# Optimization experiments

Measured on AMD Instinct MI355X. Metric: run time of the kernel, lower is better.

## Reference

```python
import jax, jax.numpy as jnp
import numpy as np

N_NODES = 50000
D = 128
N_EDGES = 600000


def setup_inputs() -> dict:
    key = jax.random.key(0)
    k_h, k_u, k_v, k_s, k_d = jax.random.split(key, 5)
    H = jax.random.normal(k_h, (N_NODES, D), dtype=jnp.float32)
    U = jax.random.normal(k_u, (D, D), dtype=jnp.float32)
    V = jax.random.normal(k_v, (D, D), dtype=jnp.float32)
    edge_src = jax.random.randint(k_s, (N_EDGES,), 0, N_NODES, dtype=jnp.int32)
    edge_dst = jax.random.randint(k_d, (N_EDGES,), 0, N_NODES, dtype=jnp.int32)
    return {"H": H, "U": U, "V": V, "edge_src": edge_src, "edge_dst": edge_dst}


def reference(H, U, V, edge_src, edge_dst):
    # Synchronous form of: new_rep[n] = relu(rep[n] @ U + sum_{m in N(n)} rep[m] @ V)
    # Compute H @ V once (one dense GEMM), then irregular gather by edge_src
    # and segment-sum scatter into destination nodes.
    hv = H @ V                                    # [N, D]
    msgs = jnp.take(hv, edge_src, axis=0)         # [E, D] irregular gather
    agg = jax.ops.segment_sum(msgs, edge_dst, num_segments=H.shape[0])  # [N, D]
    return jax.nn.relu(H @ U + agg)               # [N, D]
```

## Files before the change

### kernel.cpp

```cpp
#include <hip/hip_runtime.h>
#include <hip/hip_bf16.h>

constexpr int kNodes  = 50000;
constexpr int kEdges  = 600000;
constexpr int kD      = 128;
constexpr int kStrips = kNodes / 16;
constexpr int kStride = 64;
constexpr int kFillBlocks = (kEdges + 255) / 256;
constexpr int kPairBlocks = 2 * kFillBlocks;
constexpr int kTotalBlocks = kStrips + kFillBlocks;

typedef __attribute__((ext_vector_type(8))) short  short8;
typedef __attribute__((ext_vector_type(4))) float  f32x4;

__device__ __forceinline__ short f2bf(float x) {
    __hip_bfloat16 h = __float2bfloat16(x);
    return __builtin_bit_cast(short, h);
}

__global__ __launch_bounds__(512) void pack_init(const float* __restrict__ U,
                                                 const float* __restrict__ V,
                                                 short* __restrict__ BTf,
                                                 int* __restrict__ cursor) {
    const int g = blockIdx.x * 512 + threadIdx.x;
    if (g < 256 * kD) {
        const int c = g >> 7;
        const int k = g & 127;
        const float x = (c < kD) ? U[k * kD + c] : V[k * kD + (c - kD)];
        const int q  = c >> 6;
        const int n  = (c >> 4) & 3;
        const int m  = c & 15;
        const int t  = k >> 5;
        const int kg = (k >> 3) & 3;
        const int ko = k & 7;
        const int lane = kg * 16 + m;
        BTf[((((q * 4 + n) * 4 + t) * 64 + lane) << 3) + ko] = f2bf(x);
    }
    if (g < kNodes) cursor[g] = 0;
}

__global__ __launch_bounds__(256) void gemm_fill(const float* __restrict__ H,
                                                 const short* __restrict__ BTf,
                                                 const int* __restrict__ esrc,
                                                 const int* __restrict__ edst,
                                                 unsigned short* __restrict__ outb,
                                                 unsigned short* __restrict__ hvb,
                                                 int* __restrict__ cursor,
                                                 unsigned short* __restrict__ csr16) {
    const int bid = blockIdx.x;

    if (bid < kPairBlocks && (bid & 1)) {
        const int e = (bid >> 1) * 256 + (int)threadIdx.x;
        if (e < kEdges) {
            const int d = edst[e];
            const int slot = atomicAdd(&cursor[d], 1);
            if (slot < kStride)
                csr16[(size_t)d * kStride + slot] = (unsigned short)esrc[e];
        }
        return;
    }

    const int strip = (bid < kPairBlocks) ? (bid >> 1)
                                          : (kFillBlocks + (bid - kPairBlocks));
    const int quad  = threadIdx.x >> 6;
    const int lane  = threadIdx.x & 63;
    const int m  = lane & 15;
    const int kg = lane >> 4;
    const long row0 = (long)strip * 16;

    const float* hbase = H + (row0 + m) * kD + kg * 8;
    float4 ha[4][2];
#pragma unroll
    for (int t = 0; t < 4; ++t) {
        ha[t][0] = *reinterpret_cast<const float4*>(hbase + t * 32);
        ha[t][1] = *reinterpret_cast<const float4*>(hbase + t * 32 + 4);
    }

    const short8* bq = reinterpret_cast<const short8*>(BTf)
                     + ((size_t)quad * 16) * 64 + lane;
    short8 bf[4][4];
#pragma unroll
    for (int n = 0; n < 4; ++n)
#pragma unroll
        for (int t = 0; t < 4; ++t)
            bf[n][t] = bq[(n * 4 + t) * 64];

    short8 a[4];
#pragma unroll
    for (int t = 0; t < 4; ++t) {
        a[t][0] = f2bf(ha[t][0].x); a[t][1] = f2bf(ha[t][0].y);
        a[t][2] = f2bf(ha[t][0].z); a[t][3] = f2bf(ha[t][0].w);
        a[t][4] = f2bf(ha[t][1].x); a[t][5] = f2bf(ha[t][1].y);
        a[t][6] = f2bf(ha[t][1].z); a[t][7] = f2bf(ha[t][1].w);
    }

    f32x4 acc[4];
#pragma unroll
    for (int i = 0; i < 4; ++i) acc[i] = (f32x4){0.f, 0.f, 0.f, 0.f};
#pragma unroll
    for (int t = 0; t < 4; ++t)
#pragma unroll
        for (int n = 0; n < 4; ++n)
            acc[n] = __builtin_amdgcn_mfma_f32_16x16x32_bf16(a[t], bf[n][t], acc[n], 0, 0, 0);

    if (quad < 2) {
#pragma unroll
        for (int n = 0; n < 4; ++n) {
            const int c = quad * 64 + n * 16 + m;
#pragma unroll
            for (int j = 0; j < 4; ++j)
                outb[(size_t)(row0 + kg * 4 + j) * 256 + c] = (unsigned short)f2bf(acc[n][j]);
        }
    } else {
#pragma unroll
        for (int n = 0; n < 4; ++n) {
            const int c = (quad - 2) * 64 + n * 16 + m;
#pragma unroll
            for (int j = 0; j < 4; ++j)
                hvb[(size_t)(row0 + kg * 4 + j) * kD + c] = (unsigned short)f2bf(acc[n][j]);
        }
    }
}

__global__ __launch_bounds__(256) void aggregate_relu(const unsigned int* __restrict__ hvb,
                                                      const int* __restrict__ cursor,
                                                      const unsigned short* __restrict__ csr16,
                                                      float* __restrict__ out) {
    const int wid  = (int)((blockIdx.x * (long)blockDim.x + threadIdx.x) >> 6);
    const int lane = threadIdx.x & 63;
    if (wid >= kNodes) return;

    const int deg = min(cursor[wid], kStride);
    const unsigned int w =
        reinterpret_cast<const unsigned int*>(csr16 + (size_t)wid * kStride)[lane & 31];

    const unsigned int hw = reinterpret_cast<const unsigned int*>(out)[(size_t)wid * 128 + lane];

    float a0 = 0.f, a1 = 0.f;
    int e = 0;
    for (; e + 4 <= deg; e += 4) {
        const int p0 = __builtin_amdgcn_readlane(w, e >> 1);
        const int p1 = __builtin_amdgcn_readlane(w, (e >> 1) + 1);
        const int s0 = p0 & 0xffff, s1 = (p0 >> 16) & 0xffff;
        const int s2 = p1 & 0xffff, s3 = (p1 >> 16) & 0xffff;
        const unsigned int w0 = hvb[(size_t)s0 * 64 + lane];
        const unsigned int w1 = hvb[(size_t)s1 * 64 + lane];
        const unsigned int w2 = hvb[(size_t)s2 * 64 + lane];
        const unsigned int w3 = hvb[(size_t)s3 * 64 + lane];
        a0 += __uint_as_float(w0 << 16) + __uint_as_float(w1 << 16)
            + __uint_as_float(w2 << 16) + __uint_as_float(w3 << 16);
        a1 += __uint_as_float(w0 & 0xffff0000u) + __uint_as_float(w1 & 0xffff0000u)
            + __uint_as_float(w2 & 0xffff0000u) + __uint_as_float(w3 & 0xffff0000u);
    }
    for (; e < deg; ++e) {
        const int p = __builtin_amdgcn_readlane(w, e >> 1);
        const int s = (e & 1) ? ((p >> 16) & 0xffff) : (p & 0xffff);
        const unsigned int wv = hvb[(size_t)s * 64 + lane];
        a0 += __uint_as_float(wv << 16);
        a1 += __uint_as_float(wv & 0xffff0000u);
    }

    const float b0 = __uint_as_float(hw << 16);
    const float b1 = __uint_as_float(hw & 0xffff0000u);

    float2* out2 = reinterpret_cast<float2*>(out);
    float2 o;
    o.x = fmaxf(b0 + a0, 0.f);
    o.y = fmaxf(b1 + a1, 0.f);
    out2[(size_t)wid * 64 + lane] = o;
}

extern "C" void kernel_launch(void* const* d_in, const int* in_sizes, int n_in,
                              void* d_out, int out_size, void* d_ws, size_t ws_size,
                              hipStream_t stream) {
    const float* H    = (const float*)d_in[0];
    const float* U    = (const float*)d_in[1];
    const float* V    = (const float*)d_in[2];
    const int*   esrc = (const int*)d_in[3];
    const int*   edst = (const int*)d_in[4];

    float* out = (float*)d_out;

    char* p = (char*)d_ws;
    unsigned short* hvb  = (unsigned short*)p;  p += (size_t)kNodes * kD * 2;
    short*          BTf  = (short*)p;           p += (size_t)256 * kD * 2;
    int*            cur  = (int*)p;             p += (size_t)kNodes * 4;
    unsigned short* csr16= (unsigned short*)p;  p += (size_t)kNodes * kStride * 2;

    pack_init<<<128, 512, 0, stream>>>(U, V, BTf, cur);

    gemm_fill<<<kTotalBlocks, 256, 0, stream>>>(H, BTf, esrc, edst,
                                                (unsigned short*)d_out, hvb, cur, csr16);

    aggregate_relu<<<(kNodes * 64 + 255) / 256, 256, 0, stream>>>(
        (const unsigned int*)hvb, cur, csr16, out);
}
```

Measured before the change: 73.99 us.

## Replace per-edge global atomics with two-level bucket sort into CSR

Builds the destination-indexed adjacency in two passes. Edges are first binned into 400 coarse buckets using a shared-memory histogram and a single global atomic per bucket per block. A separate kernel then places each bucket's edges into per-node slots using shared-memory atomics. The GEMM blocks become persistent, each looping over several 16-row strips, so 768 GEMM blocks run alongside the bucketing blocks. This removes 600k scattered global atomics but adds a kernel launch and an intermediate bucket array, and it silently drops edges if a bucket exceeds 2048 entries.

```diff
diff --git a/kernel.cpp b/kernel.cpp
--- a/kernel.cpp
+++ b/kernel.cpp
@@ -6,9 +6,14 @@
 constexpr int kD      = 128;
 constexpr int kStrips = kNodes / 16;
 constexpr int kStride = 64;
-constexpr int kFillBlocks = (kEdges + 255) / 256;
-constexpr int kPairBlocks = 2 * kFillBlocks;
-constexpr int kTotalBlocks = kStrips + kFillBlocks;
+
+constexpr int kNB   = 400;
+constexpr int kNPB  = 125;
+constexpr int kCap  = 2048;
+constexpr int kEPB  = 4096;
+constexpr int kBktBlocks  = (kEdges + kEPB - 1) / kEPB;
+constexpr int kGemmBlocks = 768;
+constexpr int kTotalBlocks = kBktBlocks + kGemmBlocks;
 
 typedef __attribute__((ext_vector_type(8))) short  short8;
 typedef __attribute__((ext_vector_type(4))) float  f32x4;
@@ -21,7 +26,7 @@
 __global__ __launch_bounds__(512) void pack_init(const float* __restrict__ U,
                                                  const float* __restrict__ V,
                                                  short* __restrict__ BTf,
-                                                 int* __restrict__ cursor) {
+                                                 int* __restrict__ bcnt) {
     const int g = blockIdx.x * 512 + threadIdx.x;
     if (g < 256 * kD) {
         const int c = g >> 7;
@@ -36,45 +41,56 @@
         const int lane = kg * 16 + m;
         BTf[((((q * 4 + n) * 4 + t) * 64 + lane) << 3) + ko] = f2bf(x);
     }
-    if (g < kNodes) cursor[g] = 0;
-}
-
-__global__ __launch_bounds__(256) void gemm_fill(const float* __restrict__ H,
-                                                 const short* __restrict__ BTf,
-                                                 const int* __restrict__ esrc,
-                                                 const int* __restrict__ edst,
-                                                 unsigned short* __restrict__ outb,
-                                                 unsigned short* __restrict__ hvb,
-                                                 int* __restrict__ cursor,
-                                                 unsigned short* __restrict__ csr16) {
+    if (g < kNB * 32) bcnt[g] = 0;
+}
+
+__global__ __launch_bounds__(256) void gemm_bucket(const float* __restrict__ H,
+                                                   const short* __restrict__ BTf,
+                                                   const int* __restrict__ esrc,
+                                                   const int* __restrict__ edst,
+                                                   unsigned short* __restrict__ outb,
+                                                   unsigned short* __restrict__ hvb,
+                                                   int* __restrict__ bcnt,
+                                                   unsigned int* __restrict__ barr) {
+    __shared__ int hist[kNB];
+    __shared__ int cur[kNB];
     const int bid = blockIdx.x;
 
-    if (bid < kPairBlocks && (bid & 1)) {
-        const int e = (bid >> 1) * 256 + (int)threadIdx.x;
-        if (e < kEdges) {
-            const int d = edst[e];
-            const int slot = atomicAdd(&cursor[d], 1);
-            if (slot < kStride)
-                csr16[(size_t)d * kStride + slot] = (unsigned short)esrc[e];
+    if (bid < kBktBlocks) {
+        const int e0 = bid * kEPB;
+        for (int i = threadIdx.x; i < kNB; i += 256) hist[i] = 0;
+        __syncthreads();
+#pragma unroll
+        for (int i = 0; i < kEPB / 256; ++i) {
+            const int e = e0 + i * 256 + (int)threadIdx.x;
+            if (e < kEdges) atomicAdd(&hist[edst[e] / kNPB], 1);
+        }
+        __syncthreads();
+        for (int i = threadIdx.x; i < kNB; i += 256)
+            cur[i] = atomicAdd(&bcnt[i * 32], hist[i]);
+        __syncthreads();
+#pragma unroll
+        for (int i = 0; i < kEPB / 256; ++i) {
+            const int e = e0 + i * 256 + (int)threadIdx.x;
+            if (e < kEdges) {
+                const int d = edst[e];
+                const int b = d / kNPB;
+                const int slot = atomicAdd(&cur[b], 1);
+                if (slot < kCap)
+                    barr[(size_t)b * kCap + slot] =
+                        ((unsigned)(d - b * kNPB) << 16) | (unsigned)esrc[e];
+            }
         }
         return;
     }
 
-    const int strip = (bid < kPairBlocks) ? (bid >> 1)
-                                          : (kFillBlocks + (bid - kPairBlocks));
-    const int quad  = threadIdx.x >> 6;
-    const int lane  = threadIdx.x & 63;
+    const int g  = bid - kBktBlocks;
+    const int s0 = (int)((long)g       * kStrips / kGemmBlocks);
+    const int s1 = (int)((long)(g + 1) * kStrips / kGemmBlocks);
+    const int quad = threadIdx.x >> 6;
+    const int lane = threadIdx.x & 63;
     const int m  = lane & 15;
     const int kg = lane >> 4;
-    const long row0 = (long)strip * 16;
-
-    const float* hbase = H + (row0 + m) * kD + kg * 8;
-    float4 ha[4][2];
-#pragma unroll
-    for (int t = 0; t < 4; ++t) {
-        ha[t][0] = *reinterpret_cast<const float4*>(hbase + t * 32);
-        ha[t][1] = *reinterpret_cast<const float4*>(hbase + t * 32 + 4);
-    }
 
     const short8* bq = reinterpret_cast<const short8*>(BTf)
                      + ((size_t)quad * 16) * 64 + lane;
@@ -85,41 +101,77 @@
         for (int t = 0; t < 4; ++t)
             bf[n][t] = bq[(n * 4 + t) * 64];
 
-    short8 a[4];
-#pragma unroll
-    for (int t = 0; t < 4; ++t) {
-        a[t][0] = f2bf(ha[t][0].x); a[t][1] = f2bf(ha[t][0].y);
-        a[t][2] = f2bf(ha[t][0].z); a[t][3] = f2bf(ha[t][0].w);
-        a[t][4] = f2bf(ha[t][1].x); a[t][5] = f2bf(ha[t][1].y);
-        a[t][6] = f2bf(ha[t][1].z); a[t][7] = f2bf(ha[t][1].w);
-    }
-
-    f32x4 acc[4];
-#pragma unroll
-    for (int i = 0; i < 4; ++i) acc[i] = (f32x4){0.f, 0.f, 0.f, 0.f};
-#pragma unroll
-    for (int t = 0; t < 4; ++t)
-#pragma unroll
-        for (int n = 0; n < 4; ++n)
-            acc[n] = __builtin_amdgcn_mfma_f32_16x16x32_bf16(a[t], bf[n][t], acc[n], 0, 0, 0);
-
-    if (quad < 2) {
-#pragma unroll
-        for (int n = 0; n < 4; ++n) {
-            const int c = quad * 64 + n * 16 + m;
-#pragma unroll
-            for (int j = 0; j < 4; ++j)
-                outb[(size_t)(row0 + kg * 4 + j) * 256 + c] = (unsigned short)f2bf(acc[n][j]);
-        }
-    } else {
-#pragma unroll
-        for (int n = 0; n < 4; ++n) {
-            const int c = (quad - 2) * 64 + n * 16 + m;
-#pragma unroll
-            for (int j = 0; j < 4; ++j)
-                hvb[(size_t)(row0 + kg * 4 + j) * kD + c] = (unsigned short)f2bf(acc[n][j]);
-        }
-    }
+    for (int s = s0; s < s1; ++s) {
+        const long row0 = (long)s * 16;
+        const float* hbase = H + (row0 + m) * kD + kg * 8;
+
+        float4 ha[4][2];
+#pragma unroll
+        for (int t = 0; t < 4; ++t) {
+            ha[t][0] = *reinterpret_cast<const float4*>(hbase + t * 32);
+            ha[t][1] = *reinterpret_cast<const float4*>(hbase + t * 32 + 4);
+        }
+
+        short8 a[4];
+#pragma unroll
+        for (int t = 0; t < 4; ++t) {
+            a[t][0] = f2bf(ha[t][0].x); a[t][1] = f2bf(ha[t][0].y);
+            a[t][2] = f2bf(ha[t][0].z); a[t][3] = f2bf(ha[t][0].w);
+            a[t][4] = f2bf(ha[t][1].x); a[t][5] = f2bf(ha[t][1].y);
+            a[t][6] = f2bf(ha[t][1].z); a[t][7] = f2bf(ha[t][1].w);
+        }
+
+        f32x4 acc[4];
+#pragma unroll
+        for (int i = 0; i < 4; ++i) acc[i] = (f32x4){0.f, 0.f, 0.f, 0.f};
+#pragma unroll
+        for (int t = 0; t < 4; ++t)
+#pragma unroll
+            for (int n = 0; n < 4; ++n)
+                acc[n] = __builtin_amdgcn_mfma_f32_16x16x32_bf16(a[t], bf[n][t], acc[n], 0, 0, 0);
+
+        if (quad < 2) {
+#pragma unroll
+            for (int n = 0; n < 4; ++n) {
+                const int c = quad * 64 + n * 16 + m;
+#pragma unroll
+                for (int j = 0; j < 4; ++j)
+                    outb[(size_t)(row0 + kg * 4 + j) * 256 + c] = (unsigned short)f2bf(acc[n][j]);
+            }
+        } else {
+#pragma unroll
+            for (int n = 0; n < 4; ++n) {
+                const int c = (quad - 2) * 64 + n * 16 + m;
+#pragma unroll
+                for (int j = 0; j < 4; ++j)
+                    hvb[(size_t)(row0 + kg * 4 + j) * kD + c] = (unsigned short)f2bf(acc[n][j]);
+            }
+        }
+    }
+}
+
+__global__ __launch_bounds__(256) void bucket_sort(const int* __restrict__ bcnt,
+                                                   const unsigned int* __restrict__ barr,
+                                                   int* __restrict__ cursor,
+                                                   unsigned short* __restrict__ csr16) {
+    __shared__ int cnt[kNPB];
+    const int b = blockIdx.x;
+    for (int i = threadIdx.x; i < kNPB; i += 256) cnt[i] = 0;
+    __syncthreads();
+
+    const int n = min(bcnt[b * 32], kCap);
+    const unsigned int* arr = barr + (size_t)b * kCap;
+    for (int i = threadIdx.x; i < n; i += 256) {
+        const unsigned int p = arr[i];
+        const int dl  = (int)(p >> 16);
+        const int src = (int)(p & 0xffffu);
+        const int slot = atomicAdd(&cnt[dl], 1);
+        if (slot < kStride)
+            csr16[((size_t)b * kNPB + dl) * kStride + slot] = (unsigned short)src;
+    }
+    __syncthreads();
+    for (int i = threadIdx.x; i < kNPB; i += 256)
+        cursor[b * kNPB + i] = cnt[i];
 }
 
 __global__ __launch_bounds__(256) void aggregate_relu(const unsigned int* __restrict__ hvb,
@@ -184,14 +236,18 @@
     char* p = (char*)d_ws;
     unsigned short* hvb  = (unsigned short*)p;  p += (size_t)kNodes * kD * 2;
     short*          BTf  = (short*)p;           p += (size_t)256 * kD * 2;
-    int*            cur  = (int*)p;             p += (size_t)kNodes * 4;
-    unsigned short* csr16= (unsigned short*)p;  p += (size_t)kNodes * kStride * 2;
-
-    pack_init<<<128, 512, 0, stream>>>(U, V, BTf, cur);
-
-    gemm_fill<<<kTotalBlocks, 256, 0, stream>>>(H, BTf, esrc, edst,
-                                                (unsigned short*)d_out, hvb, cur, csr16);
+    int*            bcnt = (int*)p;             p += (size_t)kNB * 32 * 4;
+    unsigned int*   barr = (unsigned int*)p;    p += (size_t)kNB * kCap * 4;
+    int*            cursor = (int*)p;           p += (size_t)kNodes * 4;
+    unsigned short* csr16  = (unsigned short*)p;p += (size_t)kNodes * kStride * 2;
+
+    pack_init<<<128, 512, 0, stream>>>(U, V, BTf, bcnt);
+
+    gemm_bucket<<<kTotalBlocks, 256, 0, stream>>>(H, BTf, esrc, edst,
+                                                  (unsigned short*)d_out, hvb, bcnt, barr);
+
+    bucket_sort<<<kNB, 256, 0, stream>>>(bcnt, barr, cursor, csr16);
 
     aggregate_relu<<<(kNodes * 64 + 255) / 256, 256, 0, stream>>>(
-        (const unsigned int*)hvb, cur, csr16, out);
-}
+        (const unsigned int*)hvb, cursor, csr16, out);
+}
```

Result: faster. 69.39 us (-6.2%).
